# Optimization experiments

Measured on AMD Instinct MI355X. Metric: run time of the kernel, lower is better.

The kernel has to match this reference:

```python
import jax, jax.numpy as jnp
import numpy as np

B, S, D = 16, 512, 2048
NUM_HEADS, NUM_GROUPS = 16, 4
HEAD_DIM = D // NUM_HEADS  # 128
MAX_SEQ_LEN, SHARED_SLOTS = 512, 32
EPS = 1e-6


def _rope_tables(seq_positions):
    # inv_freq over half the head dim, as in the module
    inv_freq = 1.0 / (10000.0 ** (jnp.arange(0, HEAD_DIM, 2, dtype=jnp.float32) / HEAD_DIM))
    freqs = jnp.outer(seq_positions.astype(jnp.float32), inv_freq)  # [S, HEAD_DIM//2]
    return jnp.cos(freqs), jnp.sin(freqs)


def _apply_rope(x, cos, sin):
    # x: [b, s, h, head_dim]; cos/sin: [s, 1, head_dim//2] (broadcast over heads)
    x1, x2 = jnp.split(x, 2, axis=-1)
    real = x1 * cos - x2 * sin
    imag = x1 * sin + x2 * cos
    return jnp.concatenate([real, imag], axis=-1).astype(x.dtype)


def _rmsnorm(x, scale):
    # flax RMSNorm with dtype=float32: compute in fp32
    x = x.astype(jnp.float32)
    ms = jnp.mean(jnp.square(x), axis=-1, keepdims=True)
    return x * jax.lax.rsqrt(ms + EPS) * scale


def setup_inputs() -> dict:
    key = jax.random.key(0)
    ks = jax.random.split(key, 10)
    w = 0.02
    return {
        "x": jax.random.normal(ks[0], (B, S, D), dtype=jnp.float32),
        "wq": jax.random.normal(ks[1], (D, D), dtype=jnp.float32) * w,
        "bq": jnp.zeros((D,), dtype=jnp.float32),
        "wk": jax.random.normal(ks[2], (D, NUM_GROUPS * HEAD_DIM), dtype=jnp.float32) * w,
        "bk": jnp.zeros((NUM_GROUPS * HEAD_DIM,), dtype=jnp.float32),
        "wv": jax.random.normal(ks[3], (D, NUM_GROUPS * HEAD_DIM), dtype=jnp.float32) * w,
        "bv": jnp.zeros((NUM_GROUPS * HEAD_DIM,), dtype=jnp.float32),
        "wo": jax.random.normal(ks[4], (D, D), dtype=jnp.float32) * w,
        "bo": jnp.zeros((D,), dtype=jnp.float32),
        "q_norm_scale": jnp.ones((HEAD_DIM,), dtype=jnp.float32),
        "k_norm_scale": jnp.ones((HEAD_DIM,), dtype=jnp.float32),
    }


def reference(x, wq, bq, wk, bk, wv, bv, wo, bo, q_norm_scale, k_norm_scale):
    b, s, d = x.shape
    rep = NUM_HEADS // NUM_GROUPS
    head_scale = HEAD_DIM ** (-0.5)  # applied once explicitly by the module

    # nnx.Linear(dtype=float16): projections computed in fp16
    xh = x.astype(jnp.float16)
    q = (xh @ wq.astype(jnp.float16) + bq.astype(jnp.float16)).reshape(b, s, NUM_HEADS, HEAD_DIM)
    k = (xh @ wk.astype(jnp.float16) + bk.astype(jnp.float16)).reshape(b, s, NUM_GROUPS, HEAD_DIM)
    v = (xh @ wv.astype(jnp.float16) + bv.astype(jnp.float16)).reshape(b, s, NUM_GROUPS, HEAD_DIM)

    # QK RMSNorm (fp32)
    q = _rmsnorm(q, q_norm_scale)
    k = _rmsnorm(k, k_norm_scale)

    # RoPE (default positions 0..s-1)
    pos = jnp.arange(s)
    cos, sin = _rope_tables(pos)
    cos = cos[:, None, :]
    sin = sin[:, None, :]
    q = _apply_rope(q, cos, sin) * head_scale
    k = _apply_rope(k, cos, sin)

    q = q.astype(jnp.float16)
    k = k.astype(jnp.float16)
    v = v.astype(jnp.float16)

    # GQA without materializing repeated k/v: [b, s, groups, rep, head_dim]
    qg = q.reshape(b, s, NUM_GROUPS, rep, HEAD_DIM)
    # dot_product_attention applies its own 1/sqrt(head_dim) (double-scale, faithful)
    logits = jnp.einsum('btgrh,bsgh->bgrts', qg, k,
                        preferred_element_type=jnp.float32) * head_scale

    causal = pos[:, None] >= pos[None, :]  # [s, s]
    logits = jnp.where(causal[None, None, None, :, :], logits, jnp.finfo(jnp.float32).min)
    probs = jax.nn.softmax(logits, axis=-1).astype(jnp.float16)

    out = jnp.einsum('bgrts,bsgh->btgrh', probs, v)  # [b, s, groups, rep, head_dim]
    out = out.reshape(b, s, d)
    return out @ wo.astype(jnp.float16) + bo.astype(jnp.float16)
```

## Files before the change

### kernel.cpp

```cpp
#include <hip/hip_runtime.h>

#define NB 16
#define NS 512
#define ND 2048
#define NH 16
#define NG 4
#define NHD 128
#define NM (NB * NS)
#define NKD (NG * NHD)
#define NKV 1024
#define HEAD_SCALE 0.08838834764831845f

typedef _Float16 h8 __attribute__((ext_vector_type(8)));
typedef float fx4 __attribute__((ext_vector_type(4)));

__device__ __forceinline__ void gload16(const void* g, void* l) {
  __builtin_amdgcn_global_load_lds(
      (__attribute__((address_space(1))) void*)(unsigned long long)g,
      (__attribute__((address_space(3))) void*)(unsigned long long)l,
      16, 0, 0);
}


__global__ void prep_kernel(const float* __restrict__ x, _Float16* __restrict__ xh,
                            const float* __restrict__ wq, _Float16* __restrict__ wqt,
                            const float* __restrict__ wk, const float* __restrict__ wv,
                            _Float16* __restrict__ wkvt,
                            const float* __restrict__ wo, _Float16* __restrict__ wot,
                            float* __restrict__ cosT, float* __restrict__ sinT,
                            const float* __restrict__ bk, const float* __restrict__ bv,
                            float* __restrict__ bkv) {
  __shared__ float t[64][65];
  const int bid = blockIdx.x, tid = threadIdx.x;
  if (bid < 2048) {
    const fx4* p = (const fx4*)x;
    h8* o = (h8*)xh;
#pragma unroll
    for (int it = 0; it < 4; ++it) {
      int i = (it * 2048 + bid) * 256 + tid;
      fx4 a = p[2 * i], b = p[2 * i + 1];
      h8 hv;
      hv[0] = (_Float16)a[0]; hv[1] = (_Float16)a[1]; hv[2] = (_Float16)a[2]; hv[3] = (_Float16)a[3];
      hv[4] = (_Float16)b[0]; hv[5] = (_Float16)b[1]; hv[6] = (_Float16)b[2]; hv[7] = (_Float16)b[3];
      o[i] = hv;
    }
    return;
  }
  int lb = bid - 2048;
  const float* src;
  _Float16* dst;
  int K, N;
  if (lb < 1024)      { src = wq; dst = wqt; K = ND; N = ND; }
  else if (lb < 1280) { lb -= 1024; src = wk; dst = wkvt; K = ND; N = NKD; }
  else if (lb < 1536) { lb -= 1280; src = wv; dst = wkvt + (size_t)NKD * ND; K = ND; N = NKD; }
  else if (lb < 2560) { lb -= 1536; src = wo; dst = wot; K = ND; N = ND; }
  else if (lb < 2688) {
    int i = (lb - 2560) * 256 + tid;
    int s = i >> 6, f = i & 63;
    float inv = exp2f(-(float)f * (13.287712379549449f / 64.0f));
    float a = (float)s * inv;
    cosT[i] = cosf(a);
    sinT[i] = sinf(a);
    return;
  } else {
#pragma unroll
    for (int it = 0; it < 4; ++it) {
      int idx = it * 256 + tid;
      bkv[idx] = (idx < NKD) ? bk[idx] : bv[idx - NKD];
    }
    return;
  }
  const int ntil = N >> 6;
  const int n0 = (lb % ntil) * 64, k0 = (lb / ntil) * 64;
#pragma unroll
  for (int it = 0; it < 16; ++it) {
    int idx = it * 256 + tid;
    int r = idx >> 6, c = idx & 63;
    t[r][c] = src[(size_t)(k0 + r) * N + n0 + c];
  }
  __syncthreads();
#pragma unroll
  for (int it = 0; it < 16; ++it) {
    int idx = it * 256 + tid;
    int r = idx >> 6, c = idx & 63;
    dst[(size_t)(n0 + r) * K + k0 + c] = (_Float16)t[c][r];
  }
}

__global__ void vtrans_kernel(const _Float16* __restrict__ kv, _Float16* __restrict__ vt) {
  __shared__ _Float16 t[64][72];
  int st = blockIdx.x, dt = blockIdx.y, bg = blockIdx.z;
  int b = bg >> 2, g = bg & 3;
  const _Float16* src = kv + ((size_t)(b * NS + st * 64)) * NKV + NKD + g * NHD + dt * 64;
#pragma unroll
  for (int it = 0; it < 2; ++it) {
    int idx = it * 256 + threadIdx.x;
    int r = idx >> 3, c = (idx & 7) * 8;
    *(h8*)&t[r][c] = *(const h8*)(src + (size_t)r * NKV + c);
  }
  __syncthreads();
  _Float16* dst = vt + ((size_t)bg * NHD + dt * 64) * NS + st * 64;
#pragma unroll
  for (int it = 0; it < 2; ++it) {
    int idx = it * 256 + threadIdx.x;
    int r = idx >> 3, c = (idx & 7) * 8;
    h8 o;
#pragma unroll
    for (int e = 0; e < 8; ++e) o[e] = t[c + e][r];
    *(h8*)(dst + (size_t)r * NS + c) = o;
  }
}

__global__ void norm_rope_kernel(_Float16* __restrict__ Qb, _Float16* __restrict__ KVb,
                                 const float* __restrict__ qns, const float* __restrict__ kns,
                                 const float* __restrict__ cosT, const float* __restrict__ sinT) {
  int bid = blockIdx.x;
  _Float16* X;
  const float* scale;
  int hshift, rowStride;
  float outScale;
  if (bid < 32768) { X = Qb; scale = qns; hshift = 4; rowStride = ND; outScale = HEAD_SCALE; }
  else { bid -= 32768; X = KVb; scale = kns; hshift = 2; rowStride = NKV; outScale = 1.0f; }
  int wid = threadIdx.x >> 6, lane = threadIdx.x & 63;
  int task = bid * 4 + wid;
  int row = task >> hshift;
  int head = task & ((1 << hshift) - 1);
  _Float16* p = X + (size_t)row * rowStride + head * NHD;
  float x1 = (float)p[lane], x2 = (float)p[lane + 64];
  float ss = x1 * x1 + x2 * x2;
#pragma unroll
  for (int m = 1; m < 64; m <<= 1) ss += __shfl_xor(ss, m, 64);
  float rn = rsqrtf(ss * (1.0f / 128.0f) + 1e-6f);
  int s = row & (NS - 1);
  float c = cosT[s * 64 + lane], sn = sinT[s * 64 + lane];
  float n1 = x1 * rn * scale[lane], n2 = x2 * rn * scale[64 + lane];
  p[lane] = (_Float16)((n1 * c - n2 * sn) * outScale);
  p[lane + 64] = (_Float16)((n1 * sn + n2 * c) * outScale);
}

__device__ __forceinline__ void st_out(float* p, float v) { *p = v; }
__device__ __forceinline__ void st_out(_Float16* p, float v) { *p = (_Float16)v; }


template <typename OT>
__global__ __launch_bounds__(256, 3) void gemm_bt_kernel(
    const _Float16* __restrict__ A, const _Float16* __restrict__ Bt,
    const float* __restrict__ bias, OT* __restrict__ C, int N, int K) {
  __shared__ alignas(16) _Float16 As[128 * 64];
  __shared__ alignas(16) _Float16 Bs[128 * 64];
  const int tid = threadIdx.x;
  const int lane = tid & 63, wid = tid >> 6;
  const int wr = wid >> 1, wc = wid & 1;
  const int la = lane & 15, lb = (lane >> 4) * 8;
  const int bm = blockIdx.y * 128, bn = blockIdx.x * 128;

  fx4 acc[4][4] = {};

  for (int kt = 0; kt < K; kt += 64) {
    const _Float16* Ag = A + (size_t)bm * K + kt;
    const _Float16* Bg = Bt + (size_t)bn * K + kt;
#pragma unroll
    for (int it = 0; it < 4; ++it) {
      int cb = it * 256 + wid * 64;
      int ca = cb + lane;
      int r = ca >> 3, cc = ca & 7;
      gload16(Ag + (size_t)r * K + cc * 8, &As[cb * 8]);
      gload16(Bg + (size_t)r * K + cc * 8, &Bs[cb * 8]);
    }
    __syncthreads();
#pragma unroll
    for (int kk = 0; kk < 2; ++kk) {
      h8 af[4], bf[4];
#pragma unroll
      for (int m = 0; m < 4; ++m)
        af[m] = *(const h8*)&As[(wr * 64 + m * 16 + la) * 64 + kk * 32 + lb];
#pragma unroll
      for (int n = 0; n < 4; ++n)
        bf[n] = *(const h8*)&Bs[(wc * 64 + n * 16 + la) * 64 + kk * 32 + lb];
#pragma unroll
      for (int m = 0; m < 4; ++m)
#pragma unroll
        for (int n = 0; n < 4; ++n)
          acc[m][n] = __builtin_amdgcn_mfma_f32_16x16x32_f16(af[m], bf[n], acc[m][n], 0, 0, 0);
    }
    __syncthreads();
  }
#pragma unroll
  for (int m = 0; m < 4; ++m) {
    int row0 = bm + wr * 64 + m * 16 + (lane >> 4) * 4;
#pragma unroll
    for (int n = 0; n < 4; ++n) {
      int col = bn + wc * 64 + n * 16 + la;
      float bvv = bias[col];
#pragma unroll
      for (int r = 0; r < 4; ++r)
        st_out(&C[(size_t)(row0 + r) * N + col], acc[m][n][r] + bvv);
    }
  }
}


template <typename OT>
__global__ __launch_bounds__(512, 2) void gemm256_kernel(
    const _Float16* __restrict__ A, const _Float16* __restrict__ Bt,
    const float* __restrict__ bias, OT* __restrict__ C, int N, int K) {
  __shared__ alignas(16) _Float16 As[2][2][256 * 32];
  __shared__ alignas(16) _Float16 Bs[2][2][256 * 32];
  const int tid = threadIdx.x;
  const int lane = tid & 63, w = tid >> 6;
  const int wr = w >> 2, wc = w & 3;
  const int la = lane & 15, lq = lane >> 4;
  const int lin = (blockIdx.x & 7) * 32 + (blockIdx.x >> 3);
  const int nbx = N >> 8;
  const int by = lin / nbx, bx = lin % nbx;
  const int bm = by * 256, bn = bx * 256;
  const int NT = K >> 6;

  fx4 acc[8][4] = {};

  {
    const _Float16* Ag = A + (size_t)bm * K;
    const _Float16* Bg = Bt + (size_t)bn * K;
#pragma unroll
    for (int sh = 0; sh < 2; ++sh) {
#pragma unroll
      for (int i = 0; i < 2; ++i) {
        int cb = i * 512 + w * 64;
        int s = cb + lane;
        int r = s >> 2, c = s & 3;
        gload16(Ag + (size_t)r * K + sh * 32 + ((c ^ ((r >> 1) & 3)) << 3), &As[0][sh][cb * 8]);
      }
#pragma unroll
      for (int i = 0; i < 2; ++i) {
        int cb = i * 512 + w * 64;
        int s = cb + lane;
        int r = s >> 2, c = s & 3;
        gload16(Bg + (size_t)r * K + sh * 32 + ((c ^ ((r >> 1) & 3)) << 3), &Bs[0][sh][cb * 8]);
      }
    }
  }
  asm volatile("s_waitcnt vmcnt(4)" ::: "memory");
  __builtin_amdgcn_s_barrier();

  for (int kt = 0; kt < NT; ++kt) {
    const int cur = kt & 1;
    const int nxt = cur ^ 1;
    const bool more = (kt + 1 < NT);
    const _Float16* Ag = A + (size_t)bm * K + (kt + 1) * 64;
    const _Float16* Bg = Bt + (size_t)bn * K + (kt + 1) * 64;
    h8 bf[4];
#pragma unroll
    for (int ph = 0; ph < 4; ++ph) {
      const int kh = ph >> 1, g = ph & 1;
      h8 af[4];
#pragma unroll
      for (int mi = 0; mi < 4; ++mi) {
        int row = wr * 128 + (g * 4 + mi) * 16 + la;
        af[mi] = *(const h8*)&As[cur][kh][row * 32 + ((lq ^ ((row >> 1) & 3)) << 3)];
      }
      if (g == 0) {
#pragma unroll
        for (int ni = 0; ni < 4; ++ni) {
          int row = wc * 64 + ni * 16 + la;
          bf[ni] = *(const h8*)&Bs[cur][kh][row * 32 + ((lq ^ ((row >> 1) & 3)) << 3)];
        }
      }
      if (more) {
        const int sh = ph >> 1;
        const _Float16* Sg = (ph & 1) ? Bg : Ag;
        _Float16* Ld = (ph & 1) ? &Bs[nxt][sh][0] : &As[nxt][sh][0];
#pragma unroll
        for (int i = 0; i < 2; ++i) {
          int cb = i * 512 + w * 64;
          int s = cb + lane;
          int r = s >> 2, c = s & 3;
          gload16(Sg + (size_t)r * K + sh * 32 + ((c ^ ((r >> 1) & 3)) << 3), Ld + cb * 8);
        }
      }
      if (ph == 1 || ph == 3) {
        if (more) asm volatile("s_waitcnt vmcnt(4)" ::: "memory");
        else      asm volatile("s_waitcnt vmcnt(0)" ::: "memory");
      }
      __builtin_amdgcn_s_barrier();
      asm volatile("s_waitcnt lgkmcnt(0)" ::: "memory");
      __builtin_amdgcn_sched_barrier(0);
      __builtin_amdgcn_s_setprio(1);
#pragma unroll
      for (int mi = 0; mi < 4; ++mi)
#pragma unroll
        for (int ni = 0; ni < 4; ++ni)
          acc[g * 4 + mi][ni] = __builtin_amdgcn_mfma_f32_16x16x32_f16(
              af[mi], bf[ni], acc[g * 4 + mi][ni], 0, 0, 0);
      __builtin_amdgcn_s_setprio(0);
      __builtin_amdgcn_sched_barrier(0);
      __builtin_amdgcn_s_barrier();
    }
  }
#pragma unroll
  for (int mi = 0; mi < 8; ++mi) {
    int row0 = bm + wr * 128 + mi * 16 + lq * 4;
#pragma unroll
    for (int ni = 0; ni < 4; ++ni) {
      int col = bn + wc * 64 + ni * 16 + la;
      float bvv = bias[col];
#pragma unroll
      for (int r = 0; r < 4; ++r)
        st_out(&C[(size_t)(row0 + r) * N + col], acc[mi][ni][r] + bvv);
    }
  }
}


__global__ __launch_bounds__(512, 4) void attn_kernel(
    const _Float16* __restrict__ Q, const _Float16* __restrict__ KV,
    const _Float16* __restrict__ Vt, _Float16* __restrict__ ctx) {
  __shared__ alignas(16) _Float16 Ks[2][64 * 128];
  __shared__ alignas(16) _Float16 Vs[2][128 * 64];
  __shared__ alignas(16) _Float16 Ps[8][16 * 64];

  const int bid = blockIdx.x;
  const int logical = (bid & 7) * 64 + (bid >> 3);
  const int b = logical >> 5;
  const int g = (logical >> 3) & 3;
  const int jp = logical & 7;
  const int j1 = jp, j2 = 15 - jp;

  const int tid = threadIdx.x;
  const int lane = tid & 63, w = tid >> 6;
  const int la = lane & 15, lq = lane >> 4;
  const int h = g * 4 + (w & 3);
  const int rh = w >> 2;

  const _Float16* Vg = Vt + (size_t)(b * NG + g) * NHD * NS;

  auto stage = [&](int buf, int kt) {
    const _Float16* Kg = KV + ((size_t)(b * NS + kt * 64)) * NKV + g * NHD;
#pragma unroll
    for (int it = 0; it < 2; ++it) {
      int cb = it * 512 + w * 64;
      int s = cb + lane;
      int rr = s >> 4, c = s & 15;
      gload16(Kg + (size_t)rr * NKV + ((c ^ (rr & 7)) * 8), &Ks[buf][cb * 8]);
    }
#pragma unroll
    for (int it = 0; it < 2; ++it) {
      int cb = it * 512 + w * 64;
      int s = cb + lane;
      int rr = s >> 3, c = s & 7;
      gload16(Vg + (size_t)rr * NS + kt * 64 + ((c ^ (rr & 7)) * 8), &Vs[buf][cb * 8]);
    }
  };

  const int nt1 = ((j1 * 32 + 31) >> 6) + 1;
  const int nt2 = ((j2 * 32 + 31) >> 6) + 1;
  const int ntotal = nt1 + nt2;

  stage(0, 0);
  h8 qfA[4], qfB[4];
  {
    const _Float16* QgA = Q + ((size_t)(b * NS + j1 * 32 + rh * 16 + la)) * ND + h * NHD + lq * 8;
    const _Float16* QgB = Q + ((size_t)(b * NS + j2 * 32 + rh * 16 + la)) * ND + h * NHD + lq * 8;
#pragma unroll
    for (int kc = 0; kc < 4; ++kc) {
      qfA[kc] = *(const h8*)(QgA + kc * 32);
      qfB[kc] = *(const h8*)(QgB + kc * 32);
    }
  }

  fx4 oacc[8];
  float mrun[4], lrun[4];

  int cur = 0;
  for (int t = 0; t < ntotal; ++t) {
    const bool inA = t < nt1;
    const int j = inA ? j1 : j2;
    const int kt = inA ? t : t - nt1;
    const int ntj = inA ? nt1 : nt2;
    const bool more = (t + 1 < ntotal);
    if (more) {
      int nkt = (t + 1 < nt1) ? (t + 1) : (t + 1 - nt1);
      stage(cur ^ 1, nkt);
      asm volatile("s_waitcnt vmcnt(4)" ::: "memory");
    } else {
      asm volatile("s_waitcnt vmcnt(0)" ::: "memory");
    }
    __builtin_amdgcn_s_barrier();
    if (kt == 0) {
#pragma unroll
      for (int f = 0; f < 8; ++f) oacc[f] = fx4{0.f, 0.f, 0.f, 0.f};
#pragma unroll
      for (int r = 0; r < 4; ++r) { mrun[r] = -1e30f; lrun[r] = 0.f; }
    }

    fx4 sc[4] = {};
    __builtin_amdgcn_s_setprio(1);
#pragma unroll
    for (int n = 0; n < 4; ++n) {
      int row = n * 16 + la;
#pragma unroll
      for (int kc = 0; kc < 4; ++kc) {
        h8 qv = inA ? qfA[kc] : qfB[kc];
        h8 bk = *(const h8*)&Ks[cur][row * 128 + (((kc * 4 + lq) ^ (la & 7)) * 8)];
        sc[n] = __builtin_amdgcn_mfma_f32_16x16x32_f16(qv, bk, sc[n], 0, 0, 0);
      }
    }
    __builtin_amdgcn_s_setprio(0);

    const int qrow0 = j * 32 + rh * 16 + lq * 4;
    const bool maskT = (kt == ntj - 1);
    float pv[4][4];
    float rm[4] = {-1e30f, -1e30f, -1e30f, -1e30f};
#pragma unroll
    for (int n = 0; n < 4; ++n) {
      int kv = kt * 64 + n * 16 + la;
#pragma unroll
      for (int r = 0; r < 4; ++r) {
        float sv = sc[n][r] * HEAD_SCALE;
        sv = (maskT && kv > qrow0 + r) ? -1e30f : sv;
        pv[n][r] = sv;
        rm[r] = fmaxf(rm[r], sv);
      }
    }
#pragma unroll
    for (int r = 0; r < 4; ++r) {
#pragma unroll
      for (int m = 1; m < 16; m <<= 1) rm[r] = fmaxf(rm[r], __shfl_xor(rm[r], m, 64));
      float mn = fmaxf(mrun[r], rm[r]);
      float corr = __expf(mrun[r] - mn);
      mrun[r] = mn;
      lrun[r] *= corr;
#pragma unroll
      for (int f = 0; f < 8; ++f) oacc[f][r] *= corr;
    }
    float rs[4] = {0.f, 0.f, 0.f, 0.f};
#pragma unroll
    for (int n = 0; n < 4; ++n)
#pragma unroll
      for (int r = 0; r < 4; ++r) {
        float e = __expf(pv[n][r] - mrun[r]);
        pv[n][r] = e;
        rs[r] += e;
      }
#pragma unroll
    for (int r = 0; r < 4; ++r) {
#pragma unroll
      for (int m = 1; m < 16; m <<= 1) rs[r] += __shfl_xor(rs[r], m, 64);
      lrun[r] += rs[r];
    }

#pragma unroll
    for (int n = 0; n < 4; ++n)
#pragma unroll
      for (int r = 0; r < 4; ++r) {
        int row = lq * 4 + r;
        int chsw = (n * 2 + (la >> 3)) ^ (row & 7);
        Ps[w][row * 64 + chsw * 8 + (la & 7)] = (_Float16)pv[n][r];
      }
    asm volatile("s_waitcnt lgkmcnt(0)" ::: "memory");
    __builtin_amdgcn_sched_barrier(0);
    h8 pf[2];
#pragma unroll
    for (int ks = 0; ks < 2; ++ks)
      pf[ks] = *(const h8*)&Ps[w][la * 64 + (((ks * 4 + lq) ^ (la & 7)) * 8)];

    __builtin_amdgcn_s_setprio(1);
#pragma unroll
    for (int f = 0; f < 8; ++f) {
      int row = f * 16 + la;
#pragma unroll
      for (int ks = 0; ks < 2; ++ks) {
        h8 bv = *(const h8*)&Vs[cur][row * 64 + (((ks * 4 + lq) ^ (la & 7)) * 8)];
        oacc[f] = __builtin_amdgcn_mfma_f32_16x16x32_f16(pf[ks], bv, oacc[f], 0, 0, 0);
      }
    }
    __builtin_amdgcn_s_setprio(0);

    if (maskT) {
      _Float16* Cg = ctx + ((size_t)(b * NS + qrow0)) * ND + h * NHD + la;
      float inv_l[4];
#pragma unroll
      for (int r = 0; r < 4; ++r) inv_l[r] = 1.0f / lrun[r];
#pragma unroll
      for (int f = 0; f < 8; ++f)
#pragma unroll
        for (int r = 0; r < 4; ++r)
          Cg[(size_t)r * ND + f * 16] = (_Float16)(oacc[f][r] * inv_l[r]);
    }
    cur ^= 1;
  }
}


extern "C" void kernel_launch(void* const* d_in, const int* in_sizes, int n_in,
                              void* d_out, int out_size, void* d_ws, size_t ws_size,
                              hipStream_t stream) {
  (void)in_sizes; (void)n_in; (void)out_size; (void)ws_size;
  const float* x = (const float*)d_in[0];
  const float* wq = (const float*)d_in[1];
  const float* bq = (const float*)d_in[2];
  const float* wk = (const float*)d_in[3];
  const float* bk = (const float*)d_in[4];
  const float* wv = (const float*)d_in[5];
  const float* bv = (const float*)d_in[6];
  const float* wo = (const float*)d_in[7];
  const float* bo = (const float*)d_in[8];
  const float* qns = (const float*)d_in[9];
  const float* kns = (const float*)d_in[10];

  char* ws = (char*)d_ws;
  size_t off = 0;
  _Float16* xh = (_Float16*)(ws + off); off += (size_t)NM * ND * 2;
  _Float16* wqt = (_Float16*)(ws + off); off += (size_t)ND * ND * 2;
  _Float16* wkvt = (_Float16*)(ws + off); off += (size_t)NKV * ND * 2;
  _Float16* wot = (_Float16*)(ws + off); off += (size_t)ND * ND * 2;
  _Float16* Qb = (_Float16*)(ws + off); off += (size_t)NM * ND * 2;
  _Float16* KVbuf = (_Float16*)(ws + off); off += (size_t)NM * NKV * 2;
  float* cosT = (float*)(ws + off); off += (size_t)NS * 64 * 4;
  float* sinT = (float*)(ws + off); off += (size_t)NS * 64 * 4;
  float* bkv = (float*)(ws + off); off += (size_t)NKV * 4;
  _Float16* ctx = xh;
  _Float16* Vtg = wqt;

  prep_kernel<<<dim3(4737), 256, 0, stream>>>(x, xh, wq, wqt, wk, wv, wkvt, wo, wot,
                                              cosT, sinT, bk, bv, bkv);

  gemm256_kernel<_Float16><<<dim3(256), dim3(512), 0, stream>>>(xh, wqt, bq, Qb, ND, ND);
  gemm_bt_kernel<_Float16><<<dim3(NKV / 128, NM / 128), 256, 0, stream>>>(xh, wkvt, bkv, KVbuf, NKV, ND);

  norm_rope_kernel<<<dim3(40960), 256, 0, stream>>>(Qb, KVbuf, qns, kns, cosT, sinT);

  vtrans_kernel<<<dim3(NS / 64, NHD / 64, NB * NG), 256, 0, stream>>>(KVbuf, Vtg);

  attn_kernel<<<dim3(512), dim3(512), 0, stream>>>(Qb, KVbuf, Vtg, ctx);

  gemm256_kernel<float><<<dim3(256), dim3(512), 0, stream>>>(ctx, wot, bo, (float*)d_out, ND, ND);
}
```

Before: 334.7 us.

## Fuse Q RMSNorm and RoPE into attention kernel Q-fragment load

Q normalization and rotary embedding move out of the standalone norm_rope pass and into the attention kernel, which now normalizes and rotates its Q fragments in registers when each query tile starts. This removes one read-modify-write pass over the 32 MB Q buffer, and norm_rope now only processes K. The attention loop also swaps the explicit vmcnt waits plus s_barrier for a __syncthreads at the top of each iteration. That may change how prefetch overlaps with compute and could serialize the load wait differently. It also adds per-tile scalar work and cos/sin loads inside the attention kernel.

```diff
diff --git a/kernel.cpp b/kernel.cpp
--- a/kernel.cpp
+++ b/kernel.cpp
@@ -111,18 +111,11 @@
   }
 }
 
-__global__ void norm_rope_kernel(_Float16* __restrict__ Qb, _Float16* __restrict__ KVb,
-                                 const float* __restrict__ qns, const float* __restrict__ kns,
-                                 const float* __restrict__ cosT, const float* __restrict__ sinT) {
-  int bid = blockIdx.x;
-  _Float16* X;
-  const float* scale;
-  int hshift, rowStride;
-  float outScale;
-  if (bid < 32768) { X = Qb; scale = qns; hshift = 4; rowStride = ND; outScale = HEAD_SCALE; }
-  else { bid -= 32768; X = KVb; scale = kns; hshift = 2; rowStride = NKV; outScale = 1.0f; }
+__global__ void norm_rope_kernel(_Float16* __restrict__ X, const float* __restrict__ scale,
+                                 const float* __restrict__ cosT, const float* __restrict__ sinT,
+                                 int hshift, int rowStride, float outScale) {
   int wid = threadIdx.x >> 6, lane = threadIdx.x & 63;
-  int task = bid * 4 + wid;
+  int task = blockIdx.x * 4 + wid;
   int row = task >> hshift;
   int head = task & ((1 << hshift) - 1);
   _Float16* p = X + (size_t)row * rowStride + head * NHD;
@@ -313,7 +306,9 @@
 
 __global__ __launch_bounds__(512, 4) void attn_kernel(
     const _Float16* __restrict__ Q, const _Float16* __restrict__ KV,
-    const _Float16* __restrict__ Vt, _Float16* __restrict__ ctx) {
+    const _Float16* __restrict__ Vt, _Float16* __restrict__ ctx,
+    const float* __restrict__ qns, const float* __restrict__ cosT,
+    const float* __restrict__ sinT) {
   __shared__ alignas(16) _Float16 Ks[2][64 * 128];
   __shared__ alignas(16) _Float16 Vs[2][128 * 64];
   __shared__ alignas(16) _Float16 Ps[8][16 * 64];
@@ -355,37 +350,58 @@
   const int nt2 = ((j2 * 32 + 31) >> 6) + 1;
   const int ntotal = nt1 + nt2;
 
-  stage(0, 0);
-  h8 qfA[4], qfB[4];
-  {
-    const _Float16* QgA = Q + ((size_t)(b * NS + j1 * 32 + rh * 16 + la)) * ND + h * NHD + lq * 8;
-    const _Float16* QgB = Q + ((size_t)(b * NS + j2 * 32 + rh * 16 + la)) * ND + h * NHD + lq * 8;
-#pragma unroll
-    for (int kc = 0; kc < 4; ++kc) {
-      qfA[kc] = *(const h8*)(QgA + kc * 32);
-      qfB[kc] = *(const h8*)(QgB + kc * 32);
-    }
-  }
-
+  h8 qf[4];
   fx4 oacc[8];
   float mrun[4], lrun[4];
 
+  stage(0, 0);
   int cur = 0;
   for (int t = 0; t < ntotal; ++t) {
     const bool inA = t < nt1;
     const int j = inA ? j1 : j2;
     const int kt = inA ? t : t - nt1;
     const int ntj = inA ? nt1 : nt2;
-    const bool more = (t + 1 < ntotal);
-    if (more) {
+    __syncthreads();
+    if (t + 1 < ntotal) {
       int nkt = (t + 1 < nt1) ? (t + 1) : (t + 1 - nt1);
       stage(cur ^ 1, nkt);
-      asm volatile("s_waitcnt vmcnt(4)" ::: "memory");
-    } else {
-      asm volatile("s_waitcnt vmcnt(0)" ::: "memory");
-    }
-    __builtin_amdgcn_s_barrier();
+    }
     if (kt == 0) {
+      const int qrow = j * 32 + rh * 16 + la;
+      const _Float16* Qg = Q + ((size_t)(b * NS + qrow)) * ND + h * NHD + lq * 8;
+      float xq[4][8];
+      float ss = 0.f;
+#pragma unroll
+      for (int kc = 0; kc < 4; ++kc) {
+        h8 v = *(const h8*)(Qg + kc * 32);
+#pragma unroll
+        for (int e = 0; e < 8; ++e) { xq[kc][e] = (float)v[e]; ss += xq[kc][e] * xq[kc][e]; }
+      }
+      ss += __shfl_xor(ss, 16, 64);
+      ss += __shfl_xor(ss, 32, 64);
+      float rn = rsqrtf(ss * (1.0f / 128.0f) + 1e-6f);
+#pragma unroll
+      for (int kc = 0; kc < 2; ++kc) {
+        const float* s1p = qns + kc * 32 + lq * 8;
+        const float* s2p = qns + (kc + 2) * 32 + lq * 8;
+        const float* ctp = cosT + qrow * 64 + kc * 32 + lq * 8;
+        const float* stp = sinT + qrow * 64 + kc * 32 + lq * 8;
+        fx4 s1a = *(const fx4*)s1p, s1b = *(const fx4*)(s1p + 4);
+        fx4 s2a = *(const fx4*)s2p, s2b = *(const fx4*)(s2p + 4);
+        fx4 ca = *(const fx4*)ctp, cb2 = *(const fx4*)(ctp + 4);
+        fx4 sa = *(const fx4*)stp, sb = *(const fx4*)(stp + 4);
+#pragma unroll
+        for (int e = 0; e < 8; ++e) {
+          float sc1 = (e < 4) ? s1a[e & 3] : s1b[e & 3];
+          float sc2 = (e < 4) ? s2a[e & 3] : s2b[e & 3];
+          float cc = (e < 4) ? ca[e & 3] : cb2[e & 3];
+          float sn = (e < 4) ? sa[e & 3] : sb[e & 3];
+          float n1 = xq[kc][e] * rn * sc1;
+          float n2 = xq[kc + 2][e] * rn * sc2;
+          qf[kc][e] = (_Float16)((n1 * cc - n2 * sn) * HEAD_SCALE);
+          qf[kc + 2][e] = (_Float16)((n1 * sn + n2 * cc) * HEAD_SCALE);
+        }
+      }
 #pragma unroll
       for (int f = 0; f < 8; ++f) oacc[f] = fx4{0.f, 0.f, 0.f, 0.f};
 #pragma unroll
@@ -399,9 +415,8 @@
       int row = n * 16 + la;
 #pragma unroll
       for (int kc = 0; kc < 4; ++kc) {
-        h8 qv = inA ? qfA[kc] : qfB[kc];
         h8 bk = *(const h8*)&Ks[cur][row * 128 + (((kc * 4 + lq) ^ (la & 7)) * 8)];
-        sc[n] = __builtin_amdgcn_mfma_f32_16x16x32_f16(qv, bk, sc[n], 0, 0, 0);
+        sc[n] = __builtin_amdgcn_mfma_f32_16x16x32_f16(qf[kc], bk, sc[n], 0, 0, 0);
       }
     }
     __builtin_amdgcn_s_setprio(0);
@@ -527,11 +542,11 @@
   gemm256_kernel<_Float16><<<dim3(256), dim3(512), 0, stream>>>(xh, wqt, bq, Qb, ND, ND);
   gemm_bt_kernel<_Float16><<<dim3(NKV / 128, NM / 128), 256, 0, stream>>>(xh, wkvt, bkv, KVbuf, NKV, ND);
 
-  norm_rope_kernel<<<dim3(40960), 256, 0, stream>>>(Qb, KVbuf, qns, kns, cosT, sinT);
+  norm_rope_kernel<<<dim3(NM * NG / 4), 256, 0, stream>>>(KVbuf, kns, cosT, sinT, 2, NKV, 1.0f);
 
   vtrans_kernel<<<dim3(NS / 64, NHD / 64, NB * NG), 256, 0, stream>>>(KVbuf, Vtg);
 
-  attn_kernel<<<dim3(512), dim3(512), 0, stream>>>(Qb, KVbuf, Vtg, ctx);
+  attn_kernel<<<dim3(512), dim3(512), 0, stream>>>(Qb, KVbuf, Vtg, ctx, qns, cosT, sinT);
 
   gemm256_kernel<float><<<dim3(256), dim3(512), 0, stream>>>(ctx, wot, bo, (float*)d_out, ND, ND);
 }
```

After: 297.7 us. 11.0% less time.
